# Kernel optimization log

Hardware: AMD Instinct MI355X
Metric: run time of the kernel (lower is better)

Reference implementation:

```python
import jax, jax.numpy as jnp
import numpy as np

BS, SL, NN, NE = 8, 100, 200, 600
C = 110; CP1 = C + 1
D = 128          # node_embed_dim
DC = 64          # concept_embed_dim
H = 256          # lstm hidden
VOCAB = 50000
NPROB = 1000
FEAT = 2 + CP1 + DC  # LSTM input dim = 177


def setup_inputs() -> dict:
    key = jax.random.key(0)
    ks = jax.random.split(key, 24)
    f32 = jnp.float32
    p_id = jax.random.randint(ks[0], (BS, SL), 0, NPROB)
    c_id = jax.random.bernoulli(ks[1], 0.1, (BS, SL, CP1)).astype(f32)
    node_id = jax.random.randint(ks[2], (BS, SL, NN), 0, VOCAB)
    edge = jax.random.randint(ks[3], (BS, SL, 2, NE), 0, NN)
    edge_type = jax.random.randint(ks[4], (BS, SL, NE), 0, 8)
    target_c = jax.random.bernoulli(ks[5], 0.05, (BS, SL, CP1)).astype(f32)
    target_c = target_c.at[:, :, 0].set(1.0)  # every step has >=1 target concept
    result = jax.random.bernoulli(ks[6], 0.5, (BS * SL, 1)).astype(f32)
    c_embed = jax.random.bernoulli(ks[7], 0.1, (BS, SL, CP1)).astype(f32)
    cur_result = jax.random.normal(ks[8], (BS, SL, 2), f32)
    # parameters
    node_embed_w = jax.random.normal(ks[9], (VOCAB, D), f32) * 0.02
    edge_embed_w = (jax.random.normal(ks[10], (8, D), f32) * 0.02).at[0].set(0.0)  # padding_idx=0
    ggnn_w = jax.random.normal(ks[11], (4, D, D), f32) * 0.05
    gru_w_ih = jax.random.normal(ks[12], (3 * D, D), f32) * 0.05
    gru_w_hh = jax.random.normal(ks[13], (3 * D, D), f32) * 0.05
    gru_b_ih = jnp.zeros((3 * D,), f32)
    gru_b_hh = jnp.zeros((3 * D,), f32)
    transdim_w = jax.random.normal(ks[14], (DC, D), f32) * 0.05
    concept_embedding = jax.random.normal(ks[15], (CP1, DC), f32) * 0.05
    lstm_w_ih = jax.random.normal(ks[16], (4 * H, FEAT), f32) * 0.05
    lstm_w_hh = jax.random.normal(ks[17], (4 * H, H), f32) * 0.05
    lstm_b_ih = jnp.zeros((4 * H,), f32)
    lstm_b_hh = jnp.zeros((4 * H,), f32)
    pred_w = jax.random.normal(ks[18], (CP1, H), f32) * 0.05
    pred_b = jnp.zeros((CP1,), f32)
    return dict(p_id=p_id, c_id=c_id, node_id=node_id, edge=edge, edge_type=edge_type,
                target_c=target_c, result=result, c_embed=c_embed, cur_result=cur_result,
                node_embed_w=node_embed_w, edge_embed_w=edge_embed_w, ggnn_w=ggnn_w,
                gru_w_ih=gru_w_ih, gru_w_hh=gru_w_hh, gru_b_ih=gru_b_ih, gru_b_hh=gru_b_hh,
                transdim_w=transdim_w, concept_embedding=concept_embedding,
                lstm_w_ih=lstm_w_ih, lstm_w_hh=lstm_w_hh, lstm_b_ih=lstm_b_ih,
                lstm_b_hh=lstm_b_hh, pred_w=pred_w, pred_b=pred_b)


def _forward(p_id, c_id, node_id, edge, edge_type, target_c, result, c_embed, cur_result,
             node_embed_w, edge_embed_w, ggnn_w, gru_w_ih, gru_w_hh, gru_b_ih, gru_b_hh,
             transdim_w, concept_embedding, lstm_w_ih, lstm_w_hh, lstm_b_ih, lstm_b_hh,
             pred_w, pred_b):
    bs, sl = p_id.shape
    N = node_id.shape[2]
    G = bs * sl  # all graphs batched (replaces torch per-sample python loop)
    x = node_embed_w[node_id].reshape(G, N, -1)                       # [G,N,D]
    ew = edge_embed_w[edge_type].mean(-1).reshape(G, -1, 1)           # [G,E,1]
    e = edge.reshape(G, 2, -1)
    src, dst = e[:, 0], e[:, 1]                                       # [G,E]
    flat_dst = (dst + jnp.arange(G)[:, None] * N).reshape(-1)
    d = x.shape[-1]
    # GatedGraphConv, 4 layers: m = x @ W_l, sum-aggregate edge_weight*m[src] at dst, GRUCell update
    for l in range(4):
        m = jnp.einsum('gnd,de->gne', x, ggnn_w[l])
        gathered = jnp.take_along_axis(m, src[:, :, None], axis=1)    # [G,E,D]
        msg = (ew * gathered).reshape(-1, d)
        agg = jax.ops.segment_sum(msg, flat_dst, num_segments=G * N).reshape(G, N, d)
        gi = agg @ gru_w_ih.T + gru_b_ih
        gh = x @ gru_w_hh.T + gru_b_hh
        i_r, i_z, i_n = jnp.split(gi, 3, axis=-1)
        h_r, h_z, h_n = jnp.split(gh, 3, axis=-1)
        r = jax.nn.sigmoid(i_r + h_r)
        z = jax.nn.sigmoid(i_z + h_z)
        n = jnp.tanh(i_n + r * h_n)
        x = (1.0 - z) * n + z * x
    # transdim (node_embed_dim != concept_embed_dim)
    ggnn = jnp.einsum('gnd,cd->gnc', x, transdim_w)                   # [G,N,DC]
    # concept-node attention
    ce = c_embed.reshape(G, -1, 1)                                    # [G,C+1,1]
    query = ce * concept_embedding[None]                              # [G,C+1,DC]
    attn_w = jax.nn.softmax(jnp.einsum('gcd,gnd->gcn', query, ggnn), axis=2)
    attn = jnp.einsum('gcn,gnd->gcd', attn_w, ggnn) * ce
    num = jnp.sum(c_id, axis=2).reshape(G, 1)
    num = jnp.where(num == 0, 1.0, num)
    attn_out = (jnp.sum(attn, axis=1) / num).reshape(bs, sl, -1)
    # LSTM (1 layer, batch_first)
    lstm_in = jnp.concatenate([c_embed, attn_out, cur_result], axis=2)
    hdim = pred_w.shape[1]
    def step(carry, xt):
        h, c = carry
        gates = xt @ lstm_w_ih.T + lstm_b_ih + h @ lstm_w_hh.T + lstm_b_hh
        i, f, g, o = jnp.split(gates, 4, axis=-1)
        c = jax.nn.sigmoid(f) * c + jax.nn.sigmoid(i) * jnp.tanh(g)
        h = jax.nn.sigmoid(o) * jnp.tanh(c)
        return (h, c), h
    init = (jnp.zeros((bs, hdim), lstm_in.dtype), jnp.zeros((bs, hdim), lstm_in.dtype))
    _, hs = jax.lax.scan(step, init, jnp.swapaxes(lstm_in, 0, 1))
    lstm_out = jnp.swapaxes(hs, 0, 1).reshape(G, hdim)
    # prediction + masked BCE-with-logits
    pred = lstm_out @ pred_w.T + pred_b                               # [G,C+1]
    tc = target_c.reshape(G, -1)
    pred1 = jnp.sum(pred * tc, axis=1)
    nc = jnp.sum(tc, axis=1)
    mask = nc > 0
    fp = pred1 / jnp.where(mask, nc, 1.0)
    ft = result.reshape(-1)
    bce = jnp.maximum(fp, 0.0) - fp * ft + jnp.log1p(jnp.exp(-jnp.abs(fp)))
    mf = mask.astype(fp.dtype)
    loss = jnp.sum(bce * mf) / jnp.maximum(jnp.sum(mf), 1.0)
    return loss, jax.nn.sigmoid(fp), ft


def reference(p_id, c_id, node_id, edge, edge_type, target_c, result, c_embed, cur_result,
              node_embed_w, edge_embed_w, ggnn_w, gru_w_ih, gru_w_hh, gru_b_ih, gru_b_hh,
              transdim_w, concept_embedding, lstm_w_ih, lstm_w_hh, lstm_b_ih, lstm_b_hh,
              pred_w, pred_b):
    return _forward(p_id, c_id, node_id, edge, edge_type, target_c, result, c_embed, cur_result,
                    node_embed_w, edge_embed_w, ggnn_w, gru_w_ih, gru_w_hh, gru_b_ih, gru_b_hh,
                    transdim_w, concept_embedding, lstm_w_ih, lstm_w_hh, lstm_b_ih, lstm_b_hh,
                    pred_w, pred_b)
```

## Files before the change

### kernel.cpp

```cpp
#include <hip/hip_runtime.h>
#include <math.h>

static const int BSZ   = 8;
static const int SLN   = 100;
static const int NNODE = 200;
static const int NEDGE = 600;
static const int CP1N  = 111;
static const int DIM   = 128;
static const int DCN   = 64;
static const int HID   = 256;
static const int FEATN = 177;
static const int GN    = 800;
static const int MROW  = 160000;

typedef unsigned short u16;
typedef u16    u16x8  __attribute__((ext_vector_type(8)));
typedef __bf16 bf16x8 __attribute__((ext_vector_type(8)));
typedef __bf16 bf16x2 __attribute__((ext_vector_type(2)));
typedef float  f32x16 __attribute__((ext_vector_type(16)));

#if defined(__has_builtin)
# if __has_builtin(__builtin_amdgcn_fdot2_f32_bf16)
#  define HAVE_FDOT2 1
# else
#  define HAVE_FDOT2 0
# endif
# if __has_builtin(__builtin_amdgcn_exp2f)
#  define HAVE_EXP2 1
# else
#  define HAVE_EXP2 0
# endif
# if __has_builtin(__builtin_amdgcn_rcpf)
#  define HAVE_RCP 1
# else
#  define HAVE_RCP 0
# endif
#else
# define HAVE_FDOT2 0
# define HAVE_EXP2 0
# define HAVE_RCP 0
#endif

static __device__ __forceinline__ float fexp2(float x){
#if HAVE_EXP2
    return __builtin_amdgcn_exp2f(x);
#else
    return exp2f(x);
#endif
}
static __device__ __forceinline__ float frcp(float x){
#if HAVE_RCP
    return __builtin_amdgcn_rcpf(x);
#else
    return 1.f/x;
#endif
}
#define LOG2E 1.44269504088896340736f
static __device__ __forceinline__ float sigf(float v){ return frcp(1.f + fexp2(-LOG2E*v)); }
static __device__ __forceinline__ float tanh_f(float v){ return 1.f - 2.f*frcp(fexp2(2.f*LOG2E*v) + 1.f); }

__device__ __forceinline__ u16 f2bf(float f){
    union { float f; unsigned u; } v; v.f = f;
    unsigned r = v.u + 0x7FFFu + ((v.u >> 16) & 1u);
    return (u16)(r >> 16);
}
__device__ __forceinline__ float bf2f(u16 u){
    union { unsigned u; float f; } v; v.u = ((unsigned)u) << 16;
    return v.f;
}
__device__ __forceinline__ float dot2bf(unsigned w, unsigned h, float acc){
#if HAVE_FDOT2
    return __builtin_amdgcn_fdot2_f32_bf16(__builtin_bit_cast(bf16x2, w),
                                           __builtin_bit_cast(bf16x2, h), acc, false);
#else
    acc += bf2f((u16)(w & 0xffffu)) * bf2f((u16)(h & 0xffffu));
    acc += bf2f((u16)(w >> 16))     * bf2f((u16)(h >> 16));
    return acc;
#endif
}

__device__ __forceinline__ int afrag_slot(int row, int kc8){
    int kcq = kc8 >> 1;
    int pos = (row & 31) + 32*(kc8 & 1);
    return ((row >> 5)*8 + kcq)*64 + (pos ^ kcq);
}

__global__ void k_transpose_w(const float* __restrict__ whh, const float* __restrict__ wih,
                              unsigned* __restrict__ whhP, float* __restrict__ wihT){
    int idx = blockIdx.x*blockDim.x + threadIdx.x;
    const int total1 = 128*1024;
    if (idx < total1){
        int k2 = idx >> 10, j = idx & 1023;
        u16 lo = f2bf(whh[(size_t)j*256 + 2*k2]);
        u16 hi = f2bf(whh[(size_t)j*256 + 2*k2 + 1]);
        whhP[(size_t)k2*1024 + j] = (unsigned)lo | ((unsigned)hi << 16);
    }
    int idx2 = idx - total1;
    const int total2 = FEATN*1024;
    if (idx2 >= 0 && idx2 < total2){
        int k = idx2 >> 10, j = idx2 & 1023;
        wihT[(size_t)k*1024 + j] = wih[(size_t)j*FEATN + k];
    }
}

__global__ void k_convert_w(const float* __restrict__ wih, const float* __restrict__ whh,
                            const float* __restrict__ gw, const float* __restrict__ tw,
                            u16* __restrict__ wihb, u16* __restrict__ whhb,
                            u16* __restrict__ gwTb, u16* __restrict__ twb){
    int idx = blockIdx.x*blockDim.x + threadIdx.x;
    if (idx < 49152){
        wihb[idx] = f2bf(wih[idx]);
    } else if (idx < 98304){
        int t = idx - 49152;
        whhb[t] = f2bf(whh[t]);
    } else if (idx < 163840){
        int t = idx - 98304;
        int l = t >> 14, rem = t & 16383, n = rem >> 7, k = rem & 127;
        gwTb[t] = f2bf(gw[((size_t)l*128 + k)*128 + n]);
    } else if (idx < 172032){
        int t = idx - 163840;
        twb[t] = f2bf(tw[t]);
    }
}

__global__ void __launch_bounds__(256)
k_build_csr(const int* __restrict__ edge, const int* __restrict__ etype,
            const float* __restrict__ eembed,
            int* __restrict__ csr_src, float* __restrict__ csr_w, int* __restrict__ csr_off){
    int g = blockIdx.x; int tid = threadIdx.x;
    __shared__ float tmean[8];
    __shared__ float tpart[8][32];
    __shared__ int cnt[NNODE];
    __shared__ int offs[NNODE+1];
    __shared__ int cur[NNODE];
    {
        int ty = tid >> 5, lane = tid & 31;
        float s = 0.f;
        for (int i = lane; i < DIM; i += 32) s += eembed[ty*DIM + i];
        tpart[ty][lane] = s;
    }
    for (int i = tid; i < NNODE; i += 256) cnt[i] = 0;
    __syncthreads();
    if (tid < 8){
        float s = 0.f;
        for (int i = 0; i < 32; i++) s += tpart[tid][i];
        tmean[tid] = s / (float)DIM;
    }
    for (int e = tid; e < NEDGE; e += 256){
        int dst = edge[((size_t)g*2+1)*NEDGE + e];
        atomicAdd(&cnt[dst], 1);
    }
    __syncthreads();
    if (tid == 0){
        int run = 0;
        for (int i = 0; i < NNODE; i++){ offs[i] = run; run += cnt[i]; }
        offs[NNODE] = run;
    }
    __syncthreads();
    for (int i = tid; i < NNODE; i += 256) cur[i] = offs[i];
    for (int i = tid; i < NNODE+1; i += 256) csr_off[(size_t)g*(NNODE+1)+i] = offs[i];
    __syncthreads();
    for (int e = tid; e < NEDGE; e += 256){
        int dst = edge[((size_t)g*2+1)*NEDGE + e];
        int src = edge[((size_t)g*2+0)*NEDGE + e];
        float w = tmean[etype[(size_t)g*NEDGE + e]];
        int pos = atomicAdd(&cur[dst], 1);
        csr_src[(size_t)g*NEDGE + pos] = src;
        csr_w [(size_t)g*NEDGE + pos] = w;
    }
}

__global__ void k_gather_x(const int* __restrict__ nid, const float4* __restrict__ emb,
                           u16x8* __restrict__ xb){
    const long total = (long)MROW*16;
    for (long c = (long)blockIdx.x*blockDim.x + threadIdx.x; c < total; c += (long)gridDim.x*blockDim.x){
        long row = c >> 4; int p = (int)(c & 15);
        float4 a = emb[(size_t)nid[row]*32 + p*2];
        float4 b = emb[(size_t)nid[row]*32 + p*2 + 1];
        u16x8 v;
        v[0]=f2bf(a.x); v[1]=f2bf(a.y); v[2]=f2bf(a.z); v[3]=f2bf(a.w);
        v[4]=f2bf(b.x); v[5]=f2bf(b.y); v[6]=f2bf(b.z); v[7]=f2bf(b.w);
        xb[c] = v;
    }
}

__global__ void __launch_bounds__(256)
k_mm_scatter(const u16* __restrict__ xb, const u16* __restrict__ gwTb_l,
             const int* __restrict__ csr_src, const float* __restrict__ csr_w,
             const int* __restrict__ csr_off, u16* __restrict__ aggb){
    __shared__ u16 smem[224*128];
    __shared__ int   e_src[NEDGE];
    __shared__ float e_w[NEDGE];
    __shared__ int   offs_s[NNODE+1];
    int g = blockIdx.x;
    int tid = threadIdx.x;
    const u16x8* xg = (const u16x8*)(xb + (size_t)g*NNODE*DIM);
    u16x8* afrag = (u16x8*)smem;
    for (int c = tid; c < 3584; c += 256){
        int row = c >> 4, kc8 = c & 15;
        u16x8 v = {};
        if (row < NNODE) v = xg[row*16 + kc8];
        afrag[afrag_slot(row, kc8)] = v;
    }
    {
        const int*   srcp = csr_src + (size_t)g*NEDGE;
        const float* wp   = csr_w   + (size_t)g*NEDGE;
        const int*   off  = csr_off + (size_t)g*(NNODE+1);
        for (int i = tid; i < NEDGE; i += 256){ e_src[i] = srcp[i]; e_w[i] = wp[i]; }
        for (int i = tid; i <= NNODE; i += 256) offs_s[i] = off[i];
    }
    __syncthreads();
    int w = tid >> 6, lane = tid & 63;
    int nbase = w*32;
    int m = lane & 31, kh = lane >> 5;
    f32x16 acc[7];
    #pragma unroll
    for (int t = 0; t < 7; t++) acc[t] = (f32x16)0.f;
    const u16x8* bp = (const u16x8*)gwTb_l;
    int nrow = nbase + m;
    #pragma unroll
    for (int kc = 0; kc < 8; kc++){
        u16x8 b = bp[nrow*16 + kc*2 + kh];
        #pragma unroll
        for (int mt = 0; mt < 7; mt++){
            u16x8 a = afrag[(mt*8 + kc)*64 + (lane ^ kc)];
            acc[mt] = __builtin_amdgcn_mfma_f32_32x32x16_bf16(
                __builtin_bit_cast(bf16x8, a), __builtin_bit_cast(bf16x8, b), acc[mt], 0, 0, 0);
        }
    }
    __syncthreads();
    #pragma unroll
    for (int mt = 0; mt < 7; mt++){
        #pragma unroll
        for (int r = 0; r < 16; r++){
            int row = mt*32 + (r&3) + 8*(r>>2) + 4*kh;
            int col = nbase + m;
            smem[row*128 + col] = f2bf(acc[mt][r]);
        }
    }
    __syncthreads();
    const unsigned* m32 = (const unsigned*)smem;
    int j2 = tid & 63, rg = tid >> 6;
    unsigned* aggout = (unsigned*)(aggb + (size_t)g*NNODE*DIM);
    for (int i = 0; i < 50; i++){
        int n = rg*50 + i;
        int b0 = offs_s[n], e0 = offs_s[n+1];
        float a0 = 0.f, a1 = 0.f;
        for (int p = b0; p < e0; p++){
            unsigned mv = m32[e_src[p]*64 + j2];
            float w_ = e_w[p];
            a0 += w_ * bf2f((u16)(mv & 0xffffu));
            a1 += w_ * bf2f((u16)(mv >> 16));
        }
        aggout[(size_t)n*64 + j2] = (unsigned)f2bf(a0) | ((unsigned)f2bf(a1) << 16);
    }
}

__global__ void __launch_bounds__(512, 2)
k_gru_mfma(u16* __restrict__ xb, const u16* __restrict__ aggb,
           const u16* __restrict__ wihb, const u16* __restrict__ whhb,
           const float* __restrict__ bih, const float* __restrict__ bhh){
    __shared__ u16x8 afragA[2048];
    __shared__ u16x8 afragX[2048];
    int tid = threadIdx.x;
    long r0 = (long)blockIdx.x * 128;
    const u16x8* aggp = (const u16x8*)aggb;
    const u16x8* xbp  = (const u16x8*)xb;
    for (int c = tid; c < 4096; c += 512){
        int mat = c >> 11, cc = c & 2047;
        int row = cc >> 4, kc8 = cc & 15;
        u16x8 v = (mat ? xbp : aggp)[(r0 + row)*16 + kc8];
        (mat ? afragX : afragA)[afrag_slot(row, kc8)] = v;
    }
    __syncthreads();
    int w = tid >> 6, lane = tid & 63;
    int mtg = w >> 2;
    int cb  = (w & 3) * 32;
    f32x16 acc0[6], acc1[6];
    #pragma unroll
    for (int t = 0; t < 6; t++){ acc0[t] = (f32x16)0.f; acc1[t] = (f32x16)0.f; }
    const u16x8* bi = (const u16x8*)wihb;
    const u16x8* bh = (const u16x8*)whhb;
    int kh = lane >> 5;
    int ncol = cb + (lane & 31);
    #pragma unroll
    for (int kc = 0; kc < 8; kc++){
        int lx = lane ^ kc;
        u16x8 aA0 = afragA[((2*mtg+0)*8 + kc)*64 + lx];
        u16x8 aA1 = afragA[((2*mtg+1)*8 + kc)*64 + lx];
        u16x8 aX0 = afragX[((2*mtg+0)*8 + kc)*64 + lx];
        u16x8 aX1 = afragX[((2*mtg+1)*8 + kc)*64 + lx];
        #pragma unroll
        for (int g3 = 0; g3 < 3; g3++){
            int n = g3*128 + ncol;
            u16x8 b1 = bi[n*16 + kc*2 + kh];
            u16x8 b2 = bh[n*16 + kc*2 + kh];
            acc0[g3]   = __builtin_amdgcn_mfma_f32_32x32x16_bf16(
                __builtin_bit_cast(bf16x8, aA0), __builtin_bit_cast(bf16x8, b1), acc0[g3], 0,0,0);
            acc1[g3]   = __builtin_amdgcn_mfma_f32_32x32x16_bf16(
                __builtin_bit_cast(bf16x8, aA1), __builtin_bit_cast(bf16x8, b1), acc1[g3], 0,0,0);
            acc0[3+g3] = __builtin_amdgcn_mfma_f32_32x32x16_bf16(
                __builtin_bit_cast(bf16x8, aX0), __builtin_bit_cast(bf16x8, b2), acc0[3+g3], 0,0,0);
            acc1[3+g3] = __builtin_amdgcn_mfma_f32_32x32x16_bf16(
                __builtin_bit_cast(bf16x8, aX1), __builtin_bit_cast(bf16x8, b2), acc1[3+g3], 0,0,0);
        }
    }
    int col = cb + (lane & 31);
    float bir = bih[col], biz = bih[col+128], bin = bih[col+256];
    float bhr = bhh[col], bhz = bhh[col+128], bhn = bhh[col+256];
    int kc8c = col >> 3, elc = col & 7;
    #pragma unroll
    for (int mt2 = 0; mt2 < 2; mt2++){
        const f32x16* ac = mt2 ? acc1 : acc0;
        #pragma unroll
        for (int r = 0; r < 16; r++){
            int row = mtg*64 + mt2*32 + (r&3) + 8*(r>>2) + 4*kh;
            u16x8 xv = afragX[afrag_slot(row, kc8c)];
            float xo = bf2f(((const u16*)&xv)[elc]);
            float rr  = sigf(ac[0][r] + bir + ac[3][r] + bhr);
            float zz  = sigf(ac[1][r] + biz + ac[4][r] + bhz);
            float nn_ = tanh_f(ac[2][r] + bin + rr*(ac[5][r] + bhn));
            float xn  = (1.f - zz)*nn_ + zz*xo;
            xb[(size_t)(r0 + row)*DIM + col] = f2bf(xn);
        }
    }
}

__global__ void __launch_bounds__(256)
k_attention(const u16* __restrict__ xb, const u16* __restrict__ twb,
            const float* __restrict__ cemb, const float* __restrict__ cid,
            const float* __restrict__ conc, const float* __restrict__ curres,
            float* __restrict__ lstm_in){
    int g = blockIdx.x; int tid = threadIdx.x;
    int lane = tid & 63, wv = tid >> 6;
    __shared__ __align__(16) unsigned char smem_raw[57344];
    __shared__ float ce_s[CP1N];
    __shared__ float sc[256];
    __shared__ float wredA[4];
    __shared__ float wredB[4];
    __shared__ float part[4][DCN];
    __shared__ float oacc[DCN];
    __shared__ float num_s;
    u16x8* afrag = (u16x8*)smem_raw;
    float* gg    = (float*)smem_raw;
    const u16x8* xg = (const u16x8*)(xb + (size_t)g*NNODE*DIM);
    for (int c = tid; c < 3584; c += 256){
        int row = c >> 4, kc8 = c & 15;
        u16x8 v = {};
        if (row < NNODE) v = xg[row*16 + kc8];
        afrag[afrag_slot(row, kc8)] = v;
    }
    if (tid < CP1N) ce_s[tid] = cemb[(size_t)g*CP1N + tid];
    if (tid < DCN) oacc[tid] = 0.f;
    {
        float v = (tid < CP1N) ? cid[(size_t)g*CP1N + tid] : 0.f;
        #pragma unroll
        for (int m2 = 32; m2; m2 >>= 1) v += __shfl_xor(v, m2);
        if (lane == 0) wredA[wv] = v;
    }
    __syncthreads();
    if (tid == 0){
        float nm = wredA[0]+wredA[1]+wredA[2]+wredA[3];
        num_s = (nm == 0.f) ? 1.f : nm;
    }
    {
        int ct = wv & 1, rh = wv >> 1;
        int tb = rh ? 4 : 0;
        int ntile = rh ? 3 : 4;
        int m = lane & 31, kh = lane >> 5;
        f32x16 acc[4];
        #pragma unroll
        for (int t = 0; t < 4; t++) acc[t] = (f32x16)0.f;
        const u16x8* tp = (const u16x8*)twb;
        #pragma unroll
        for (int kc = 0; kc < 8; kc++){
            u16x8 b = tp[(ct*32 + m)*16 + kc*2 + kh];
            #pragma unroll
            for (int t = 0; t < 4; t++){
                if (t < ntile){
                    u16x8 a = afrag[((tb+t)*8 + kc)*64 + (lane ^ kc)];
                    acc[t] = __builtin_amdgcn_mfma_f32_32x32x16_bf16(
                        __builtin_bit_cast(bf16x8, a), __builtin_bit_cast(bf16x8, b), acc[t], 0,0,0);
                }
            }
        }
        __syncthreads();
        #pragma unroll
        for (int t = 0; t < 4; t++){
            if (t < ntile){
                #pragma unroll
                for (int r = 0; r < 16; r++){
                    int row = (tb+t)*32 + (r&3) + 8*(r>>2) + 4*kh;
                    int col = ct*32 + m;
                    if (row < NNODE) gg[row*65 + col] = acc[t][r];
                }
            }
        }
    }
    __syncthreads();
    for (int c = 0; c < CP1N; c++){
        float ce = ce_s[c];
        if (ce == 0.f) continue;
        const float* qc = conc + c*DCN;
        float s = -1e30f;
        if (tid < NNODE){
            float a_ = 0.f;
            const float* gr_ = &gg[tid*65];
            #pragma unroll 16
            for (int d = 0; d < DCN; d++) a_ += qc[d] * gr_[d];
            s = ce * a_;
        }
        float m_ = s;
        #pragma unroll
        for (int m2 = 32; m2; m2 >>= 1) m_ = fmaxf(m_, __shfl_xor(m_, m2));
        if (lane == 0) wredA[wv] = m_;
        __syncthreads();
        float mx = fmaxf(fmaxf(wredA[0], wredA[1]), fmaxf(wredA[2], wredA[3]));
        float e = (tid < NNODE) ? fexp2(LOG2E*(s - mx)) : 0.f;
        sc[tid] = e;
        float sum_ = e;
        #pragma unroll
        for (int m2 = 32; m2; m2 >>= 1) sum_ += __shfl_xor(sum_, m2);
        if (lane == 0) wredB[wv] = sum_;
        __syncthreads();
        float inv = ce / (wredB[0]+wredB[1]+wredB[2]+wredB[3]);
        float pa = 0.f;
        for (int n = wv; n < NNODE; n += 4) pa += sc[n] * gg[n*65 + lane];
        part[wv][lane] = pa;
        __syncthreads();
        if (tid < DCN) oacc[tid] += inv * (part[0][tid] + part[1][tid] + part[2][tid] + part[3][tid]);
    }
    __syncthreads();
    if (tid < FEATN){
        float v;
        if      (tid < CP1N)       v = ce_s[tid];
        else if (tid < CP1N+DCN)   v = oacc[tid-CP1N] / num_s;
        else                       v = curres[(size_t)g*2 + (tid-CP1N-DCN)];
        lstm_in[(size_t)g*FEATN + tid] = v;
    }
}

__global__ void __launch_bounds__(256)
k_gi(const float* __restrict__ lstm_in, const float* __restrict__ wihT,
     const float* __restrict__ bih, const float* __restrict__ bhh, float* __restrict__ gi){
    int rb = blockIdx.x;
    int jb = blockIdx.y;
    int tid = threadIdx.x;
    __shared__ float in_s[8][FEATN];
    for (int i = tid; i < 8*FEATN; i += 256){ int r = i/FEATN, k = i%FEATN; in_s[r][k] = lstm_in[((size_t)rb*8+r)*FEATN + k]; }
    __syncthreads();
    int j = jb*256 + tid;
    float acc[8];
    #pragma unroll
    for (int i = 0; i < 8; i++) acc[i] = 0.f;
    for (int k = 0; k < FEATN; k++){
        float w = wihT[(size_t)k*1024 + j];
        #pragma unroll
        for (int i = 0; i < 8; i++) acc[i] += in_s[i][k] * w;
    }
    float b = bih[j] + bhh[j];
    #pragma unroll
    for (int i = 0; i < 8; i++) gi[((size_t)rb*8+i)*1024 + j] = acc[i] + b;
}

static const int WREG = 104;
static const int WL4  = 6;

__global__ void __launch_bounds__(1024)
__attribute__((amdgpu_waves_per_eu(4,4)))
k_lstm(const float* __restrict__ gi, const unsigned* __restrict__ whhP, float* __restrict__ out){
    int b = blockIdx.x; int tid = threadIdx.x;
    __shared__ uint4 ldsw4[WL4][1024];
    __shared__ float gates[1024];
    __shared__ __align__(8) u16 h16[HID];
    unsigned wreg[WREG];
    #pragma unroll
    for (int i = 0; i < WREG; i++) wreg[i] = whhP[(size_t)i*1024 + tid];
    #pragma unroll
    for (int q = 0; q < WL4; q++){
        uint4 v;
        v.x = whhP[(size_t)(WREG + 4*q + 0)*1024 + tid];
        v.y = whhP[(size_t)(WREG + 4*q + 1)*1024 + tid];
        v.z = whhP[(size_t)(WREG + 4*q + 2)*1024 + tid];
        v.w = whhP[(size_t)(WREG + 4*q + 3)*1024 + tid];
        ldsw4[q][tid] = v;
    }
    if (tid < 128) ((unsigned*)h16)[tid] = 0u;
    float c_reg = 0.f;
    int lane = tid & 63;
    __syncthreads();
    float giv = gi[(size_t)b*SLN*1024 + tid];
    for (int t = 0; t < SLN; t++){
        unsigned hv0 = ((const unsigned*)h16)[lane];
        unsigned hv1 = ((const unsigned*)h16)[64 + lane];
        float acc0 = giv, acc1 = 0.f;
        if (t+1 < SLN) giv = gi[((size_t)b*SLN + t + 1)*1024 + tid];
        #pragma unroll
        for (int p = 0; p < 64; p += 2){
            unsigned hpa = (unsigned)__builtin_amdgcn_readlane((int)hv0, p);
            unsigned hpb = (unsigned)__builtin_amdgcn_readlane((int)hv0, p+1);
            acc0 = dot2bf(wreg[p],   hpa, acc0);
            acc1 = dot2bf(wreg[p+1], hpb, acc1);
        }
        #pragma unroll
        for (int p = 64; p < WREG; p += 2){
            unsigned hpa = (unsigned)__builtin_amdgcn_readlane((int)hv1, p - 64);
            unsigned hpb = (unsigned)__builtin_amdgcn_readlane((int)hv1, p - 63);
            acc0 = dot2bf(wreg[p],   hpa, acc0);
            acc1 = dot2bf(wreg[p+1], hpb, acc1);
        }
        #pragma unroll
        for (int q = 0; q < WL4; q++){
            uint4 wv = ldsw4[q][tid];
            int base = WREG + 4*q - 64;
            unsigned h0 = (unsigned)__builtin_amdgcn_readlane((int)hv1, base + 0);
            unsigned h1 = (unsigned)__builtin_amdgcn_readlane((int)hv1, base + 1);
            unsigned h2 = (unsigned)__builtin_amdgcn_readlane((int)hv1, base + 2);
            unsigned h3 = (unsigned)__builtin_amdgcn_readlane((int)hv1, base + 3);
            acc0 = dot2bf(wv.x, h0, acc0);
            acc1 = dot2bf(wv.y, h1, acc1);
            acc0 = dot2bf(wv.z, h2, acc0);
            acc1 = dot2bf(wv.w, h3, acc1);
        }
        gates[tid] = acc0 + acc1;
        __syncthreads();
        if (tid < HID){
            float i_ = sigf(gates[tid]);
            float f_ = sigf(gates[tid+256]);
            float g_ = tanh_f(gates[tid+512]);
            float o_ = sigf(gates[tid+768]);
            c_reg = f_*c_reg + i_*g_;
            float h = o_*tanh_f(c_reg);
            out[((size_t)b*SLN + t)*HID + tid] = h;
            h16[tid] = f2bf(h);
        }
        __syncthreads();
    }
}

__global__ void __launch_bounds__(128)
k_final(const float* __restrict__ lstm_out, const float* __restrict__ pw, const float* __restrict__ pb,
        const float* __restrict__ tc, const float* __restrict__ result,
        float* __restrict__ out, float* __restrict__ lacc){
    int row = blockIdx.x; int tid = threadIdx.x;
    __shared__ __align__(16) float h_s[HID];
    __shared__ float redv[128], redn[128];
    h_s[tid]       = lstm_out[(size_t)row*HID + tid];
    h_s[tid + 128] = lstm_out[(size_t)row*HID + tid + 128];
    __syncthreads();
    float v = 0.f, n = 0.f;
    if (tid < CP1N){
        float acc = pb[tid];
        const float4* wr = (const float4*)(pw + (size_t)tid*HID);
        const float4* hp = (const float4*)h_s;
        #pragma unroll 8
        for (int k4 = 0; k4 < 64; k4++){
            float4 w = wr[k4]; float4 h4 = hp[k4];
            acc += h4.x*w.x + h4.y*w.y + h4.z*w.z + h4.w*w.w;
        }
        float t = tc[(size_t)row*CP1N + tid];
        v = acc*t; n = t;
    }
    redv[tid] = v; redn[tid] = n;
    __syncthreads();
    for (int s = 64; s > 0; s >>= 1){
        if (tid < s){ redv[tid] += redv[tid+s]; redn[tid] += redn[tid+s]; }
        __syncthreads();
    }
    if (tid == 0){
        float nc = redn[0];
        bool mask = nc > 0.f;
        float fp = redv[0] / (mask ? nc : 1.f);
        float ft = result[row];
        float bce = fmaxf(fp, 0.f) - fp*ft + log1pf(expf(-fabsf(fp)));
        out[1 + row]      = 1.f/(1.f + expf(-fp));
        out[1 + GN + row] = ft;
        if (mask){ atomicAdd(&lacc[0], bce); atomicAdd(&lacc[1], 1.f); }
    }
}

__global__ void k_loss_final(const float* __restrict__ lacc, float* __restrict__ out){
    out[0] = lacc[0] / fmaxf(lacc[1], 1.f);
}

extern "C" void kernel_launch(void* const* d_in, const int* in_sizes, int n_in,
                              void* d_out, int out_size, void* d_ws, size_t ws_size,
                              hipStream_t stream) {
    const float* c_id        = (const float*)d_in[1];
    const int*   node_id     = (const int*)  d_in[2];
    const int*   edge        = (const int*)  d_in[3];
    const int*   etype       = (const int*)  d_in[4];
    const float* target_c    = (const float*)d_in[5];
    const float* result      = (const float*)d_in[6];
    const float* c_embed     = (const float*)d_in[7];
    const float* cur_result  = (const float*)d_in[8];
    const float* node_emb_w  = (const float*)d_in[9];
    const float* edge_emb_w  = (const float*)d_in[10];
    const float* ggnn_w      = (const float*)d_in[11];
    const float* gru_w_ih    = (const float*)d_in[12];
    const float* gru_w_hh    = (const float*)d_in[13];
    const float* gru_b_ih    = (const float*)d_in[14];
    const float* gru_b_hh    = (const float*)d_in[15];
    const float* transdim_w  = (const float*)d_in[16];
    const float* concept     = (const float*)d_in[17];
    const float* lstm_w_ih   = (const float*)d_in[18];
    const float* lstm_w_hh   = (const float*)d_in[19];
    const float* lstm_b_ih   = (const float*)d_in[20];
    const float* lstm_b_hh   = (const float*)d_in[21];
    const float* pred_w      = (const float*)d_in[22];
    const float* pred_b      = (const float*)d_in[23];
    float* out = (float*)d_out;

    char* ws = (char*)d_ws;
    size_t off = 0;
    auto alloc = [&](size_t bytes) -> void* {
        void* p = ws + off;
        off += (bytes + 255) & ~(size_t)255;
        return p;
    };
    u16*      xb       = (u16*)     alloc((size_t)MROW*DIM*2);
    u16*      aggb     = (u16*)     alloc((size_t)MROW*DIM*2);
    int*      csr_src  = (int*)     alloc((size_t)GN*NEDGE*4);
    float*    csr_w    = (float*)   alloc((size_t)GN*NEDGE*4);
    int*      csr_off  = (int*)     alloc((size_t)GN*(NNODE+1)*4);
    float*    lstm_in  = (float*)   alloc((size_t)GN*FEATN*4);
    float*    gi       = (float*)   alloc((size_t)GN*1024*4);
    unsigned* whhP     = (unsigned*)alloc((size_t)128*1024*4);
    float*    wihT     = (float*)   alloc((size_t)FEATN*1024*4);
    float*    lstm_out = (float*)   alloc((size_t)GN*HID*4);
    u16*      wihb     = (u16*)     alloc((size_t)384*128*2);
    u16*      whhb     = (u16*)     alloc((size_t)384*128*2);
    u16*      gwTb     = (u16*)     alloc((size_t)4*128*128*2);
    u16*      twb      = (u16*)     alloc((size_t)DCN*DIM*2);
    float*    lacc     = (float*)   alloc(256);

    hipMemsetAsync(lacc, 0, 8, stream);
    {
        int total = 128*1024 + FEATN*1024;
        k_transpose_w<<<(total + 255)/256, 256, 0, stream>>>(lstm_w_hh, lstm_w_ih, whhP, wihT);
    }
    k_convert_w<<<672, 256, 0, stream>>>(gru_w_ih, gru_w_hh, ggnn_w, transdim_w, wihb, whhb, gwTb, twb);
    k_build_csr<<<GN, 256, 0, stream>>>(edge, etype, edge_emb_w, csr_src, csr_w, csr_off);
    k_gather_x<<<4096, 256, 0, stream>>>(node_id, (const float4*)node_emb_w, (u16x8*)xb);
    for (int l = 0; l < 4; l++){
        k_mm_scatter<<<GN, 256, 0, stream>>>(xb, gwTb + (size_t)l*DIM*DIM,
                                             csr_src, csr_w, csr_off, aggb);
        k_gru_mfma<<<MROW/128, 512, 0, stream>>>(xb, aggb, wihb, whhb, gru_b_ih, gru_b_hh);
    }
    k_attention<<<GN, 256, 0, stream>>>(xb, twb, c_embed, c_id, concept, cur_result, lstm_in);
    k_gi<<<dim3(100, 4), 256, 0, stream>>>(lstm_in, wihT, lstm_b_ih, lstm_b_hh, gi);
    k_lstm<<<BSZ, 1024, 0, stream>>>(gi, whhP, lstm_out);
    k_final<<<GN, 128, 0, stream>>>(lstm_out, pred_w, pred_b, target_c, result, out, lacc);
    k_loss_final<<<1, 1, 0, stream>>>(lacc, out);
}
```

Measured before the change: 1.189 ms.

## Fuse embedding gather into first GGNN layer and batch attention over four concepts

Drops the separate embedding-gather kernel. The first layer's scatter and GRU kernels now read node embeddings directly and convert them to bf16, which avoids writing and re-reading the bf16 node-feature buffer once. The attention kernel compacts the active concepts into a list and handles four at a time, so each block pays one set of barriers per four concepts instead of one per concept, at the cost of more shared memory. The first-layer kernels now gather the embeddings twice (once in scatter, once in GRU), which adds redundant random reads.

New measurement: 1.123 ms, median of 2. 5.5% less time.

```diff
diff --git a/kernel.cpp b/kernel.cpp
--- a/kernel.cpp
+++ b/kernel.cpp
@@ -85,6 +85,15 @@
     return ((row >> 5)*8 + kcq)*64 + (pos ^ kcq);
 }
 
+__device__ __forceinline__ u16x8 pack_emb(const float4* __restrict__ emb, int id, int kc8){
+    float4 a = emb[(size_t)id*32 + kc8*2];
+    float4 b = emb[(size_t)id*32 + kc8*2 + 1];
+    u16x8 v;
+    v[0]=f2bf(a.x); v[1]=f2bf(a.y); v[2]=f2bf(a.z); v[3]=f2bf(a.w);
+    v[4]=f2bf(b.x); v[5]=f2bf(b.y); v[6]=f2bf(b.z); v[7]=f2bf(b.w);
+    return v;
+}
+
 __global__ void k_transpose_w(const float* __restrict__ whh, const float* __restrict__ wih,
                               unsigned* __restrict__ whhP, float* __restrict__ wihT){
     int idx = blockIdx.x*blockDim.x + threadIdx.x;
@@ -170,37 +179,33 @@
     }
 }
 
-__global__ void k_gather_x(const int* __restrict__ nid, const float4* __restrict__ emb,
-                           u16x8* __restrict__ xb){
-    const long total = (long)MROW*16;
-    for (long c = (long)blockIdx.x*blockDim.x + threadIdx.x; c < total; c += (long)gridDim.x*blockDim.x){
-        long row = c >> 4; int p = (int)(c & 15);
-        float4 a = emb[(size_t)nid[row]*32 + p*2];
-        float4 b = emb[(size_t)nid[row]*32 + p*2 + 1];
-        u16x8 v;
-        v[0]=f2bf(a.x); v[1]=f2bf(a.y); v[2]=f2bf(a.z); v[3]=f2bf(a.w);
-        v[4]=f2bf(b.x); v[5]=f2bf(b.y); v[6]=f2bf(b.z); v[7]=f2bf(b.w);
-        xb[c] = v;
-    }
-}
-
 __global__ void __launch_bounds__(256)
 k_mm_scatter(const u16* __restrict__ xb, const u16* __restrict__ gwTb_l,
              const int* __restrict__ csr_src, const float* __restrict__ csr_w,
-             const int* __restrict__ csr_off, u16* __restrict__ aggb){
+             const int* __restrict__ csr_off, u16* __restrict__ aggb,
+             const float4* __restrict__ emb, const int* __restrict__ nid, int first){
     __shared__ u16 smem[224*128];
     __shared__ int   e_src[NEDGE];
     __shared__ float e_w[NEDGE];
     __shared__ int   offs_s[NNODE+1];
     int g = blockIdx.x;
     int tid = threadIdx.x;
-    const u16x8* xg = (const u16x8*)(xb + (size_t)g*NNODE*DIM);
     u16x8* afrag = (u16x8*)smem;
-    for (int c = tid; c < 3584; c += 256){
-        int row = c >> 4, kc8 = c & 15;
-        u16x8 v = {};
-        if (row < NNODE) v = xg[row*16 + kc8];
-        afrag[afrag_slot(row, kc8)] = v;
+    if (first){
+        for (int c = tid; c < 3584; c += 256){
+            int row = c >> 4, kc8 = c & 15;
+            u16x8 v = {};
+            if (row < NNODE) v = pack_emb(emb, nid[(size_t)g*NNODE + row], kc8);
+            afrag[afrag_slot(row, kc8)] = v;
+        }
+    } else {
+        const u16x8* xg = (const u16x8*)(xb + (size_t)g*NNODE*DIM);
+        for (int c = tid; c < 3584; c += 256){
+            int row = c >> 4, kc8 = c & 15;
+            u16x8 v = {};
+            if (row < NNODE) v = xg[row*16 + kc8];
+            afrag[afrag_slot(row, kc8)] = v;
+        }
     }
     {
         const int*   srcp = csr_src + (size_t)g*NEDGE;
@@ -259,18 +264,30 @@
 __global__ void __launch_bounds__(512, 2)
 k_gru_mfma(u16* __restrict__ xb, const u16* __restrict__ aggb,
            const u16* __restrict__ wihb, const u16* __restrict__ whhb,
-           const float* __restrict__ bih, const float* __restrict__ bhh){
+           const float* __restrict__ bih, const float* __restrict__ bhh,
+           const float4* __restrict__ emb, const int* __restrict__ nid, int first){
     __shared__ u16x8 afragA[2048];
     __shared__ u16x8 afragX[2048];
     int tid = threadIdx.x;
     long r0 = (long)blockIdx.x * 128;
     const u16x8* aggp = (const u16x8*)aggb;
-    const u16x8* xbp  = (const u16x8*)xb;
-    for (int c = tid; c < 4096; c += 512){
-        int mat = c >> 11, cc = c & 2047;
-        int row = cc >> 4, kc8 = cc & 15;
-        u16x8 v = (mat ? xbp : aggp)[(r0 + row)*16 + kc8];
-        (mat ? afragX : afragA)[afrag_slot(row, kc8)] = v;
+    if (first){
+        for (int c = tid; c < 2048; c += 512){
+            int row = c >> 4, kc8 = c & 15;
+            afragX[afrag_slot(row, kc8)] = pack_emb(emb, nid[r0 + row], kc8);
+        }
+        for (int c = tid; c < 2048; c += 512){
+            int row = c >> 4, kc8 = c & 15;
+            afragA[afrag_slot(row, kc8)] = aggp[(r0 + row)*16 + kc8];
+        }
+    } else {
+        const u16x8* xbp = (const u16x8*)xb;
+        for (int c = tid; c < 4096; c += 512){
+            int mat = c >> 11, cc = c & 2047;
+            int row = cc >> 4, kc8 = cc & 15;
+            u16x8 v = (mat ? xbp : aggp)[(r0 + row)*16 + kc8];
+            (mat ? afragX : afragA)[afrag_slot(row, kc8)] = v;
+        }
     }
     __syncthreads();
     int w = tid >> 6, lane = tid & 63;
@@ -335,12 +352,14 @@
     int lane = tid & 63, wv = tid >> 6;
     __shared__ __align__(16) unsigned char smem_raw[57344];
     __shared__ float ce_s[CP1N];
-    __shared__ float sc[256];
-    __shared__ float wredA[4];
-    __shared__ float wredB[4];
-    __shared__ float part[4][DCN];
+    __shared__ float sc4[4][256];
+    __shared__ float wredA[4][4];
+    __shared__ float wredB[4][4];
+    __shared__ float part4[4][4][DCN];
     __shared__ float oacc[DCN];
     __shared__ float num_s;
+    __shared__ int actv[CP1N];
+    __shared__ int nact_s;
     u16x8* afrag = (u16x8*)smem_raw;
     float* gg    = (float*)smem_raw;
     const u16x8* xg = (const u16x8*)(xb + (size_t)g*NNODE*DIM);
@@ -350,18 +369,23 @@
         if (row < NNODE) v = xg[row*16 + kc8];
         afrag[afrag_slot(row, kc8)] = v;
     }
+    if (tid == 0) nact_s = 0;
     if (tid < CP1N) ce_s[tid] = cemb[(size_t)g*CP1N + tid];
     if (tid < DCN) oacc[tid] = 0.f;
     {
         float v = (tid < CP1N) ? cid[(size_t)g*CP1N + tid] : 0.f;
         #pragma unroll
         for (int m2 = 32; m2; m2 >>= 1) v += __shfl_xor(v, m2);
-        if (lane == 0) wredA[wv] = v;
+        if (lane == 0) wredA[wv][0] = v;
     }
     __syncthreads();
     if (tid == 0){
-        float nm = wredA[0]+wredA[1]+wredA[2]+wredA[3];
+        float nm = wredA[0][0]+wredA[1][0]+wredA[2][0]+wredA[3][0];
         num_s = (nm == 0.f) ? 1.f : nm;
+    }
+    if (tid < CP1N && ce_s[tid] != 0.f){
+        int p = atomicAdd(&nact_s, 1);
+        actv[p] = tid;
     }
     {
         int ct = wv & 1, rh = wv >> 1;
@@ -398,37 +422,77 @@
         }
     }
     __syncthreads();
-    for (int c = 0; c < CP1N; c++){
-        float ce = ce_s[c];
-        if (ce == 0.f) continue;
-        const float* qc = conc + c*DCN;
-        float s = -1e30f;
+    int nact = nact_s;
+    for (int ci = 0; ci < nact; ci += 4){
+        int i0 = actv[ci];
+        int i1 = actv[(ci+1 < nact) ? ci+1 : nact-1];
+        int i2 = actv[(ci+2 < nact) ? ci+2 : nact-1];
+        int i3 = actv[(ci+3 < nact) ? ci+3 : nact-1];
+        float ce0 = ce_s[i0], ce1 = ce_s[i1], ce2 = ce_s[i2], ce3 = ce_s[i3];
+        const float* q0 = conc + i0*DCN;
+        const float* q1 = conc + i1*DCN;
+        const float* q2 = conc + i2*DCN;
+        const float* q3 = conc + i3*DCN;
+        float s0=-1e30f, s1=-1e30f, s2=-1e30f, s3=-1e30f;
         if (tid < NNODE){
-            float a_ = 0.f;
+            float a0=0.f,a1=0.f,a2=0.f,a3=0.f;
             const float* gr_ = &gg[tid*65];
-            #pragma unroll 16
-            for (int d = 0; d < DCN; d++) a_ += qc[d] * gr_[d];
-            s = ce * a_;
-        }
-        float m_ = s;
-        #pragma unroll
-        for (int m2 = 32; m2; m2 >>= 1) m_ = fmaxf(m_, __shfl_xor(m_, m2));
-        if (lane == 0) wredA[wv] = m_;
+            #pragma unroll 8
+            for (int d = 0; d < DCN; d++){
+                float gv = gr_[d];
+                a0 += q0[d]*gv; a1 += q1[d]*gv; a2 += q2[d]*gv; a3 += q3[d]*gv;
+            }
+            s0 = ce0*a0; s1 = ce1*a1; s2 = ce2*a2; s3 = ce3*a3;
+        }
+        float m0=s0, m1=s1, m2=s2, m3=s3;
+        #pragma unroll
+        for (int mk = 32; mk; mk >>= 1){
+            m0 = fmaxf(m0, __shfl_xor(m0, mk));
+            m1 = fmaxf(m1, __shfl_xor(m1, mk));
+            m2 = fmaxf(m2, __shfl_xor(m2, mk));
+            m3 = fmaxf(m3, __shfl_xor(m3, mk));
+        }
+        if (lane == 0){ wredA[wv][0]=m0; wredA[wv][1]=m1; wredA[wv][2]=m2; wredA[wv][3]=m3; }
         __syncthreads();
-        float mx = fmaxf(fmaxf(wredA[0], wredA[1]), fmaxf(wredA[2], wredA[3]));
-        float e = (tid < NNODE) ? fexp2(LOG2E*(s - mx)) : 0.f;
-        sc[tid] = e;
-        float sum_ = e;
-        #pragma unroll
-        for (int m2 = 32; m2; m2 >>= 1) sum_ += __shfl_xor(sum_, m2);
-        if (lane == 0) wredB[wv] = sum_;
+        float mx0 = fmaxf(fmaxf(wredA[0][0],wredA[1][0]), fmaxf(wredA[2][0],wredA[3][0]));
+        float mx1 = fmaxf(fmaxf(wredA[0][1],wredA[1][1]), fmaxf(wredA[2][1],wredA[3][1]));
+        float mx2 = fmaxf(fmaxf(wredA[0][2],wredA[1][2]), fmaxf(wredA[2][2],wredA[3][2]));
+        float mx3 = fmaxf(fmaxf(wredA[0][3],wredA[1][3]), fmaxf(wredA[2][3],wredA[3][3]));
+        float e0 = (tid < NNODE) ? fexp2(LOG2E*(s0-mx0)) : 0.f;
+        float e1 = (tid < NNODE) ? fexp2(LOG2E*(s1-mx1)) : 0.f;
+        float e2 = (tid < NNODE) ? fexp2(LOG2E*(s2-mx2)) : 0.f;
+        float e3 = (tid < NNODE) ? fexp2(LOG2E*(s3-mx3)) : 0.f;
+        sc4[0][tid]=e0; sc4[1][tid]=e1; sc4[2][tid]=e2; sc4[3][tid]=e3;
+        float u0=e0,u1=e1,u2=e2,u3=e3;
+        #pragma unroll
+        for (int mk = 32; mk; mk >>= 1){
+            u0 += __shfl_xor(u0, mk);
+            u1 += __shfl_xor(u1, mk);
+            u2 += __shfl_xor(u2, mk);
+            u3 += __shfl_xor(u3, mk);
+        }
+        if (lane == 0){ wredB[wv][0]=u0; wredB[wv][1]=u1; wredB[wv][2]=u2; wredB[wv][3]=u3; }
         __syncthreads();
-        float inv = ce / (wredB[0]+wredB[1]+wredB[2]+wredB[3]);
-        float pa = 0.f;
-        for (int n = wv; n < NNODE; n += 4) pa += sc[n] * gg[n*65 + lane];
-        part[wv][lane] = pa;
+        float inv0 = ce0 / (wredB[0][0]+wredB[1][0]+wredB[2][0]+wredB[3][0]);
+        float inv1 = (ci+1 < nact) ? ce1 / (wredB[0][1]+wredB[1][1]+wredB[2][1]+wredB[3][1]) : 0.f;
+        float inv2 = (ci+2 < nact) ? ce2 / (wredB[0][2]+wredB[1][2]+wredB[2][2]+wredB[3][2]) : 0.f;
+        float inv3 = (ci+3 < nact) ? ce3 / (wredB[0][3]+wredB[1][3]+wredB[2][3]+wredB[3][3]) : 0.f;
+        float pa0=0.f, pa1=0.f, pa2=0.f, pa3=0.f;
+        for (int n = wv; n < NNODE; n += 4){
+            float gv = gg[n*65 + lane];
+            pa0 += sc4[0][n]*gv; pa1 += sc4[1][n]*gv;
+            pa2 += sc4[2][n]*gv; pa3 += sc4[3][n]*gv;
+        }
+        part4[wv][0][lane]=pa0; part4[wv][1][lane]=pa1;
+        part4[wv][2][lane]=pa2; part4[wv][3][lane]=pa3;
         __syncthreads();
-        if (tid < DCN) oacc[tid] += inv * (part[0][tid] + part[1][tid] + part[2][tid] + part[3][tid]);
+        if (tid < DCN){
+            float t0 = part4[0][0][tid]+part4[1][0][tid]+part4[2][0][tid]+part4[3][0][tid];
+            float t1 = part4[0][1][tid]+part4[1][1][tid]+part4[2][1][tid]+part4[3][1][tid];
+            float t2 = part4[0][2][tid]+part4[1][2][tid]+part4[2][2][tid]+part4[3][2][tid];
+            float t3 = part4[0][3][tid]+part4[1][3][tid]+part4[2][3][tid]+part4[3][3][tid];
+            oacc[tid] += inv0*t0 + inv1*t1 + inv2*t2 + inv3*t3;
+        }
     }
     __syncthreads();
     if (tid < FEATN){
@@ -641,11 +705,12 @@
     }
     k_convert_w<<<672, 256, 0, stream>>>(gru_w_ih, gru_w_hh, ggnn_w, transdim_w, wihb, whhb, gwTb, twb);
     k_build_csr<<<GN, 256, 0, stream>>>(edge, etype, edge_emb_w, csr_src, csr_w, csr_off);
-    k_gather_x<<<4096, 256, 0, stream>>>(node_id, (const float4*)node_emb_w, (u16x8*)xb);
     for (int l = 0; l < 4; l++){
         k_mm_scatter<<<GN, 256, 0, stream>>>(xb, gwTb + (size_t)l*DIM*DIM,
-                                             csr_src, csr_w, csr_off, aggb);
-        k_gru_mfma<<<MROW/128, 512, 0, stream>>>(xb, aggb, wihb, whhb, gru_b_ih, gru_b_hh);
+                                             csr_src, csr_w, csr_off, aggb,
+                                             (const float4*)node_emb_w, node_id, l == 0);
+        k_gru_mfma<<<MROW/128, 512, 0, stream>>>(xb, aggb, wihb, whhb, gru_b_ih, gru_b_hh,
+                                                 (const float4*)node_emb_w, node_id, l == 0);
     }
     k_attention<<<GN, 256, 0, stream>>>(xb, twb, c_embed, c_id, concept, cur_result, lstm_in);
     k_gi<<<dim3(100, 4), 256, 0, stream>>>(lstm_in, wihT, lstm_b_ih, lstm_b_hh, gi);
```
